# Kernel tuning notes

Measured on AMD Instinct MI355X. Metric: run time of the kernel, lower is better.

The kernel has to match this reference:

```python
import jax, jax.numpy as jnp
import numpy as np

H = 256          # hidden_size
V_IN = 29        # in_embeddng_size
V_OUT = 74       # out_embedding_size
L = 32           # encoder sequence length
STEPS = 20       # max_decoding_steps
BOS, EOS = 2, 3


def gru_cell(x, h, Wih, Whh, bih, bhh):
    # torch GRU cell: r,z,n gate order in the stacked [3H, H] weight matrices
    gi = x @ Wih.T + bih          # [3H]
    gh = h @ Whh.T + bhh          # [3H]
    ir, iz, inn = jnp.split(gi, 3)
    hr, hz, hn = jnp.split(gh, 3)
    r = jax.nn.sigmoid(ir + hr)
    z = jax.nn.sigmoid(iz + hz)
    n = jnp.tanh(inn + r * hn)
    return (1.0 - z) * n + z * h


def setup_inputs() -> dict:
    key = jax.random.key(0)
    ks = jax.random.split(key, 14)
    f = lambda k, shape: (jax.random.normal(k, shape, jnp.float32) * 0.08)
    inp = {
        "enc_input": jax.random.randint(ks[0], (1, L), 0, V_IN).astype(jnp.int32),
        "enc_emb": f(ks[1], (V_IN, H)).at[0].set(0.0),   # padding_idx=0
        "enc_Wih": f(ks[2], (3 * H, H)),
        "enc_Whh": f(ks[3], (3 * H, H)),
        "enc_bih": f(ks[4], (3 * H,)),
        "enc_bhh": f(ks[5], (3 * H,)),
        "dec_emb": f(ks[6], (V_OUT, H)).at[0].set(0.0),  # padding_idx=0
        "dec_Wih": f(ks[7], (3 * H, H)),
        "dec_Whh": f(ks[8], (3 * H, H)),
        "dec_bih": f(ks[9], (3 * H,)),
        "dec_bhh": f(ks[10], (3 * H,)),
        "fc_W": f(ks[11], (V_OUT, H)),
        "fc_b": f(ks[12], (V_OUT,)),
    }
    return inp


def reference(enc_input, enc_emb, enc_Wih, enc_Whh, enc_bih, enc_bhh,
              dec_emb, dec_Wih, dec_Whh, dec_bih, dec_bhh, fc_W, fc_b):
    # ---- encoder: embed + single-layer GRU over the sequence (batch=1) ----
    x_seq = enc_emb[enc_input[0]]                     # [L, H]
    def enc_step(h, x):
        return gru_cell(x, h, enc_Wih, enc_Whh, enc_bih, enc_bhh), None
    h0 = jnp.zeros((H,), enc_emb.dtype)
    h, _ = jax.lax.scan(enc_step, h0, x_seq)          # final hidden [H]

    # Early break is emulated by a `done` flag: once EOS is emitted, all
    # subsequent preds stay 0 (matching torch, which leaves preds zeros).
    def dec_step(carry, _):
        h, tok, done = carry
        x = dec_emb[tok]
        h2 = gru_cell(x, h, dec_Wih, dec_Whh, dec_bih, dec_bhh)
        logit = h2 @ fc_W.T + fc_b                    # [V_OUT]
        topi = jnp.argmax(logit).astype(jnp.int32)    # topk(1) == argmax
        is_eos = topi == EOS
        pred = jnp.where(done | is_eos, 0, topi)      # EOS step not recorded
        return (h2, topi, done | is_eos), pred

    init = (h, jnp.int32(BOS), jnp.bool_(False))
    _, preds = jax.lax.scan(dec_step, init, None, length=STEPS)
    return preds                                      # [20] int32
```

## Files before the change

### kernel.cpp

```cpp
#include <hip/hip_runtime.h>
#include <cmath>

#define H     256
#define H3    768
#define L     32
#define STEPS 20
#define VOUT  74
#define NWG   16
#define HW    16
#define ROWS  48
#define NITEMS (L + VOUT)

#define WS_HW    64
#define WS_EGI   1088
#define WS_DGI   (1088 + L * H3)

__device__ __forceinline__ float sigmoidf_(float x) {
    return 1.0f / (1.0f + expf(-x));
}

__device__ __forceinline__ int growf(int w, int lr) {
    int j = w * HW + (lr & 15);
    return (lr < 16) ? j : (lr < 32 ? H + j : 2 * H + j);
}

__global__ void prep(const int*   __restrict__ enc_input,
                     const float* __restrict__ enc_emb,
                     const float* __restrict__ encWih,
                     const float* __restrict__ enc_bih,
                     const float* __restrict__ dec_emb,
                     const float* __restrict__ decWih,
                     const float* __restrict__ dec_bih,
                     float* __restrict__ ws) {
    if (blockIdx.x == 0) {
        for (int k = threadIdx.x; k < 1088; k += 256) ((int*)ws)[k] = 0;
    }
    int wid  = blockIdx.x * 4 + (threadIdx.x >> 6);
    int lane = threadIdx.x & 63;
    if (wid >= NITEMS * H3) return;
    int item = wid / H3;
    int j    = wid - item * H3;

    const float* x; const float* W; const float* b; float* out;
    if (item < L) {
        x = enc_emb + enc_input[item] * H;  W = encWih + j * H;
        b = enc_bih;                        out = ws + WS_EGI + item * H3 + j;
    } else {
        int v = item - L;
        x = dec_emb + v * H;                W = decWih + j * H;
        b = dec_bih;                        out = ws + WS_DGI + v * H3 + j;
    }
    float4 w  = ((const float4*)W)[lane];
    float4 xv = ((const float4*)x)[lane];
    float s = fmaf(w.x, xv.x, fmaf(w.y, xv.y, fmaf(w.z, xv.z, w.w * xv.w)));
    #pragma unroll
    for (int m = 1; m < 64; m <<= 1) s += __shfl_xor(s, m);
    if (lane == 0) *out = s + b[j];
}

__global__ __launch_bounds__(256, 1) void gru_seq(
        const float* __restrict__ enc_Whh, const float* __restrict__ enc_bhh,
        const float* __restrict__ dec_Whh, const float* __restrict__ dec_bhh,
        const float* __restrict__ fc_W,    const float* __restrict__ fc_b,
        float* __restrict__ ws, int* __restrict__ out) {
    __shared__ float hl[1040];
    __shared__ float fcL[VOUT * 260];
    __shared__ float fb[VOUT];
    __shared__ float gh_l[ROWS];
    __shared__ float gi_l[ROWS];
    __shared__ float log_l[VOUT];
    __shared__ int   s_tok, s_done;

    const int t = threadIdx.x;
    const int w = blockIdx.x;
    unsigned long long* hw = (unsigned long long*)(ws + WS_HW);

    if (t == 0) { s_done = 0; s_tok = 2; }
    if (w == 0 && t < STEPS) out[t] = 0;
    for (int idx = t; idx < VOUT * H; idx += 256)
        fcL[(idx >> 8) * 260 + (idx & 255)] = fc_W[idx];
    if (t < VOUT) fb[t] = fc_b[t];

    const int p  = t & 3;
    const int lr = t >> 2;
    const int g  = growf(w, lr < ROWS ? lr : 0);
    float4 wE[16], wD[16];
    float bhhE = 0.f, bhhD = 0.f;
    if (t < 4 * ROWS) {
        const float* eb = enc_Whh + g * H + p * 64;
        const float* db = dec_Whh + g * H + p * 64;
        #pragma unroll
        for (int i = 0; i < 16; ++i) {
            wE[i] = *(const float4*)(eb + 4 * i);
            wD[i] = *(const float4*)(db + 4 * i);
        }
        if (p == 0) { bhhE = enc_bhh[g]; bhhD = dec_bhh[g]; }
    }

    int tok = 2;
    for (int s = 0; s <= L + STEPS; ++s) {
        {
            unsigned long long u;
            const unsigned long long* src = hw + (s & 1) * H + t;
            do {
                u = __hip_atomic_load(src, __ATOMIC_RELAXED,
                                      __HIP_MEMORY_SCOPE_AGENT);
            } while ((unsigned)u != (unsigned)s);
            float hv = __uint_as_float((unsigned)(u >> 32));
            hl[t] = hv; hl[260 + t] = hv; hl[520 + t] = hv; hl[780 + t] = hv;
        }
        __syncthreads();

        if (s >= L + 1) {
            const int G = t >> 4, li = t & 15;
            const float* hb2 = hl + (li & 3) * 260 + li * 16;
            #pragma unroll
            for (int m = 0; m < 5; ++m) {
                int r = G + (m << 4);
                if (r < VOUT) {
                    const float* fr = fcL + r * 260 + li * 16;
                    float a = 0.f;
                    #pragma unroll
                    for (int c = 0; c < 4; ++c) {
                        float4 f  = *(const float4*)(fr + 4 * c);
                        float4 h4 = *(const float4*)(hb2 + 4 * c);
                        a = fmaf(f.x, h4.x, fmaf(f.y, h4.y,
                              fmaf(f.z, h4.z, fmaf(f.w, h4.w, a))));
                    }
                    a += __shfl_xor(a, 1); a += __shfl_xor(a, 2);
                    a += __shfl_xor(a, 4); a += __shfl_xor(a, 8);
                    if (li == 0) log_l[r] = a + fb[r];
                }
            }
            __syncthreads();
            if (t < 64) {
                float v = log_l[t]; int bi = t;
                if (t < VOUT - 64) {
                    float v2 = log_l[64 + t];
                    if (v2 > v) { v = v2; bi = 64 + t; }
                }
                #pragma unroll
                for (int m = 1; m < 64; m <<= 1) {
                    float ov = __shfl_xor(v, m);
                    int   ob = __shfl_xor(bi, m);
                    if (ov > v || (ov == v && ob < bi)) { v = ov; bi = ob; }
                }
                if (t == 0) {
                    bool eos = (bi == 3);
                    if (w == 0 && !eos) out[s - (L + 1)] = bi;
                    s_tok = bi;
                    if (eos) s_done = 1;
                }
            }
            __syncthreads();
            tok = s_tok;
            if (s_done || s == L + STEPS) break;
        }

        if (t < 4 * ROWS) {
            float acc = (s < L) ? bhhE : bhhD;
            const float* hb = hl + p * 324;
            if (s < L) {
                #pragma unroll
                for (int i = 0; i < 16; ++i) {
                    float4 h4 = *(const float4*)(hb + 4 * i);
                    acc = fmaf(wE[i].x, h4.x, fmaf(wE[i].y, h4.y,
                          fmaf(wE[i].z, h4.z, fmaf(wE[i].w, h4.w, acc))));
                }
            } else {
                #pragma unroll
                for (int i = 0; i < 16; ++i) {
                    float4 h4 = *(const float4*)(hb + 4 * i);
                    acc = fmaf(wD[i].x, h4.x, fmaf(wD[i].y, h4.y,
                          fmaf(wD[i].z, h4.z, fmaf(wD[i].w, h4.w, acc))));
                }
            }
            acc += __shfl_xor(acc, 1);
            acc += __shfl_xor(acc, 2);
            if (p == 0) gh_l[lr] = acc;
        } else if (t - 4 * ROWS < ROWS) {
            int lr2 = t - 4 * ROWS;
            const float* gib = (s < L) ? (ws + WS_EGI + s * H3)
                                       : (ws + WS_DGI + tok * H3);
            gi_l[lr2] = gib[growf(w, lr2)];
        }
        __syncthreads();

        if (t < HW) {
            int gj = w * HW + t;
            float r = sigmoidf_(gi_l[t]      + gh_l[t]);
            float z = sigmoidf_(gi_l[16 + t] + gh_l[16 + t]);
            float n = tanhf    (gi_l[32 + t] + r * gh_l[32 + t]);
            float hn = (1.f - z) * n + z * hl[gj];
            unsigned long long pk =
                ((unsigned long long)__float_as_uint(hn) << 32) |
                (unsigned)(s + 1);
            __hip_atomic_store(hw + ((s + 1) & 1) * H + gj, pk,
                               __ATOMIC_RELAXED, __HIP_MEMORY_SCOPE_AGENT);
        }
    }
}

extern "C" void kernel_launch(void* const* d_in, const int* in_sizes, int n_in,
                              void* d_out, int out_size, void* d_ws, size_t ws_size,
                              hipStream_t stream) {
    const int*   enc_input = (const int*)  d_in[0];
    const float* enc_emb   = (const float*)d_in[1];
    const float* enc_Wih   = (const float*)d_in[2];
    const float* enc_Whh   = (const float*)d_in[3];
    const float* enc_bih   = (const float*)d_in[4];
    const float* enc_bhh   = (const float*)d_in[5];
    const float* dec_emb   = (const float*)d_in[6];
    const float* dec_Wih   = (const float*)d_in[7];
    const float* dec_Whh   = (const float*)d_in[8];
    const float* dec_bih   = (const float*)d_in[9];
    const float* dec_bhh   = (const float*)d_in[10];
    const float* fc_W      = (const float*)d_in[11];
    const float* fc_b      = (const float*)d_in[12];
    float* ws  = (float*)d_ws;
    int*  outp = (int*)d_out;

    hipLaunchKernelGGL(prep, dim3((NITEMS * H3 + 3) / 4), dim3(256), 0, stream,
                       enc_input, enc_emb, enc_Wih, enc_bih,
                       dec_emb, dec_Wih, dec_bih, ws);
    hipLaunchKernelGGL(gru_seq, dim3(NWG), dim3(256), 0, stream,
                       enc_Whh, enc_bhh, dec_Whh, dec_bhh, fc_W, fc_b,
                       ws, outp);
}
```

Before: 141.8 us.

## Keep FC weights in registers, preload input gates to LDS, pad hidden exchange slots

Each thread now holds its fc_W rows in registers, replacing the LDS copy of the whole matrix. The per-block slices of the precomputed input-gate projections for every encoder step and every decoder token go into LDS once, so no global read remains inside the step loop. Warp 0 now runs the argmax in parallel with the recurrent matvec done by the other warps, which removes one barrier per decoder step. Each hidden-exchange slot is padded to 64 bytes to reduce false sharing between polling blocks, at the cost of much higher register pressure (wE, wD and wF arrays) and a larger workspace clear.

```diff
diff --git a/kernel.cpp b/kernel.cpp
--- a/kernel.cpp
+++ b/kernel.cpp
@@ -11,9 +11,9 @@
 #define ROWS  48
 #define NITEMS (L + VOUT)
 
-#define WS_HW    64
-#define WS_EGI   1088
-#define WS_DGI   (1088 + L * H3)
+#define WS_HX    0
+#define WS_EGI   8192
+#define WS_DGI   (8192 + L * H3)
 
 __device__ __forceinline__ float sigmoidf_(float x) {
     return 1.0f / (1.0f + expf(-x));
@@ -33,7 +33,7 @@
                      const float* __restrict__ dec_bih,
                      float* __restrict__ ws) {
     if (blockIdx.x == 0) {
-        for (int k = threadIdx.x; k < 1088; k += 256) ((int*)ws)[k] = 0;
+        for (int k = threadIdx.x; k < 8192; k += 256) ((int*)ws)[k] = 0;
     }
     int wid  = blockIdx.x * 4 + (threadIdx.x >> 6);
     int lane = threadIdx.x & 63;
@@ -63,30 +63,37 @@
         const float* __restrict__ dec_Whh, const float* __restrict__ dec_bhh,
         const float* __restrict__ fc_W,    const float* __restrict__ fc_b,
         float* __restrict__ ws, int* __restrict__ out) {
-    __shared__ float hl[1040];
-    __shared__ float fcL[VOUT * 260];
+    __shared__ __align__(16) float hl[1040];
     __shared__ float fb[VOUT];
     __shared__ float gh_l[ROWS];
-    __shared__ float gi_l[ROWS];
+    __shared__ float egi_l[L * ROWS];
+    __shared__ float dgi_l[VOUT * ROWS];
     __shared__ float log_l[VOUT];
     __shared__ int   s_tok, s_done;
 
     const int t = threadIdx.x;
     const int w = blockIdx.x;
-    unsigned long long* hw = (unsigned long long*)(ws + WS_HW);
+    unsigned long long* hx = (unsigned long long*)(ws + WS_HX);
 
     if (t == 0) { s_done = 0; s_tok = 2; }
     if (w == 0 && t < STEPS) out[t] = 0;
-    for (int idx = t; idx < VOUT * H; idx += 256)
-        fcL[(idx >> 8) * 260 + (idx & 255)] = fc_W[idx];
     if (t < VOUT) fb[t] = fc_b[t];
-
+    for (int idx = t; idx < L * ROWS; idx += 256) {
+        int item = idx / ROWS, lr = idx - item * ROWS;
+        egi_l[idx] = ws[WS_EGI + item * H3 + growf(w, lr)];
+    }
+    for (int idx = t; idx < VOUT * ROWS; idx += 256) {
+        int item = idx / ROWS, lr = idx - item * ROWS;
+        dgi_l[idx] = ws[WS_DGI + item * H3 + growf(w, lr)];
+    }
+
+    const int m  = t - 64;
     const int p  = t & 3;
-    const int lr = t >> 2;
-    const int g  = growf(w, lr < ROWS ? lr : 0);
+    const int lr = (t >= 64) ? (m >> 2) : 0;
+    const int g  = growf(w, lr);
     float4 wE[16], wD[16];
     float bhhE = 0.f, bhhD = 0.f;
-    if (t < 4 * ROWS) {
+    if (t >= 64) {
         const float* eb = enc_Whh + g * H + p * 64;
         const float* db = dec_Whh + g * H + p * 64;
         #pragma unroll
@@ -97,11 +104,24 @@
         if (p == 0) { bhhE = enc_bhh[g]; bhhD = dec_bhh[g]; }
     }
 
+    const int rF = t >> 2;
+    float4 wF[16], wF2[16];
+    {
+        const float* fp = fc_W + rF * H + p * 64;
+        #pragma unroll
+        for (int i = 0; i < 16; ++i) wF[i] = *(const float4*)(fp + 4 * i);
+        if (t < 40) {
+            const float* fp2 = fc_W + (64 + rF) * H + p * 64;
+            #pragma unroll
+            for (int i = 0; i < 16; ++i) wF2[i] = *(const float4*)(fp2 + 4 * i);
+        }
+    }
+
     int tok = 2;
     for (int s = 0; s <= L + STEPS; ++s) {
         {
+            const unsigned long long* src = hx + ((unsigned)((s & 1) * H + t)) * 8;
             unsigned long long u;
-            const unsigned long long* src = hw + (s & 1) * H + t;
             do {
                 u = __hip_atomic_load(src, __ATOMIC_RELAXED,
                                       __HIP_MEMORY_SCOPE_AGENT);
@@ -111,38 +131,43 @@
         }
         __syncthreads();
 
-        if (s >= L + 1) {
-            const int G = t >> 4, li = t & 15;
-            const float* hb2 = hl + (li & 3) * 260 + li * 16;
+        const bool dec_out = (s >= L + 1);
+        if (dec_out) {
+            const float* hb = hl + p * 324;
+            float a = 0.f;
             #pragma unroll
-            for (int m = 0; m < 5; ++m) {
-                int r = G + (m << 4);
-                if (r < VOUT) {
-                    const float* fr = fcL + r * 260 + li * 16;
-                    float a = 0.f;
-                    #pragma unroll
-                    for (int c = 0; c < 4; ++c) {
-                        float4 f  = *(const float4*)(fr + 4 * c);
-                        float4 h4 = *(const float4*)(hb2 + 4 * c);
-                        a = fmaf(f.x, h4.x, fmaf(f.y, h4.y,
-                              fmaf(f.z, h4.z, fmaf(f.w, h4.w, a))));
-                    }
-                    a += __shfl_xor(a, 1); a += __shfl_xor(a, 2);
-                    a += __shfl_xor(a, 4); a += __shfl_xor(a, 8);
-                    if (li == 0) log_l[r] = a + fb[r];
-                }
+            for (int i = 0; i < 16; ++i) {
+                float4 h4 = *(const float4*)(hb + 4 * i);
+                a = fmaf(wF[i].x, h4.x, fmaf(wF[i].y, h4.y,
+                      fmaf(wF[i].z, h4.z, fmaf(wF[i].w, h4.w, a))));
+            }
+            a += __shfl_xor(a, 1); a += __shfl_xor(a, 2);
+            if (p == 0) log_l[rF] = a + fb[rF];
+            if (t < 40) {
+                float a2 = 0.f;
+                #pragma unroll
+                for (int i = 0; i < 16; ++i) {
+                    float4 h4 = *(const float4*)(hb + 4 * i);
+                    a2 = fmaf(wF2[i].x, h4.x, fmaf(wF2[i].y, h4.y,
+                           fmaf(wF2[i].z, h4.z, fmaf(wF2[i].w, h4.w, a2))));
+                }
+                a2 += __shfl_xor(a2, 1); a2 += __shfl_xor(a2, 2);
+                if (p == 0) log_l[64 + rF] = a2 + fb[64 + rF];
             }
             __syncthreads();
-            if (t < 64) {
+        }
+
+        if (t < 64) {
+            if (dec_out) {
                 float v = log_l[t]; int bi = t;
                 if (t < VOUT - 64) {
                     float v2 = log_l[64 + t];
                     if (v2 > v) { v = v2; bi = 64 + t; }
                 }
                 #pragma unroll
-                for (int m = 1; m < 64; m <<= 1) {
-                    float ov = __shfl_xor(v, m);
-                    int   ob = __shfl_xor(bi, m);
+                for (int mm = 1; mm < 64; mm <<= 1) {
+                    float ov = __shfl_xor(v, mm);
+                    int   ob = __shfl_xor(bi, mm);
                     if (ov > v || (ov == v && ob < bi)) { v = ov; bi = ob; }
                 }
                 if (t == 0) {
@@ -152,12 +177,7 @@
                     if (eos) s_done = 1;
                 }
             }
-            __syncthreads();
-            tok = s_tok;
-            if (s_done || s == L + STEPS) break;
-        }
-
-        if (t < 4 * ROWS) {
+        } else {
             float acc = (s < L) ? bhhE : bhhD;
             const float* hb = hl + p * 324;
             if (s < L) {
@@ -177,26 +197,26 @@
             }
             acc += __shfl_xor(acc, 1);
             acc += __shfl_xor(acc, 2);
-            if (p == 0) gh_l[lr] = acc;
-        } else if (t - 4 * ROWS < ROWS) {
-            int lr2 = t - 4 * ROWS;
-            const float* gib = (s < L) ? (ws + WS_EGI + s * H3)
-                                       : (ws + WS_DGI + tok * H3);
-            gi_l[lr2] = gib[growf(w, lr2)];
+            if (p == 0) gh_l[m >> 2] = acc;
         }
         __syncthreads();
 
+        if (dec_out) {
+            tok = s_tok;
+            if (s_done || s == L + STEPS) break;
+        }
+
         if (t < HW) {
-            int gj = w * HW + t;
-            float r = sigmoidf_(gi_l[t]      + gh_l[t]);
-            float z = sigmoidf_(gi_l[16 + t] + gh_l[16 + t]);
-            float n = tanhf    (gi_l[32 + t] + r * gh_l[32 + t]);
-            float hn = (1.f - z) * n + z * hl[gj];
+            const float* gi = (s < L) ? (egi_l + s * ROWS) : (dgi_l + tok * ROWS);
+            float r = sigmoidf_(gi[t]      + gh_l[t]);
+            float z = sigmoidf_(gi[16 + t] + gh_l[16 + t]);
+            float n = tanhf    (gi[32 + t] + r * gh_l[32 + t]);
+            float hn = (1.f - z) * n + z * hl[w * HW + t];
             unsigned long long pk =
                 ((unsigned long long)__float_as_uint(hn) << 32) |
                 (unsigned)(s + 1);
-            __hip_atomic_store(hw + ((s + 1) & 1) * H + gj, pk,
-                               __ATOMIC_RELAXED, __HIP_MEMORY_SCOPE_AGENT);
+            __hip_atomic_store(hx + ((unsigned)(((s + 1) & 1) * H + w * HW + t)) * 8,
+                               pk, __ATOMIC_RELAXED, __HIP_MEMORY_SCOPE_AGENT);
         }
     }
 }
```

New measurement: 153.8 us. 1.08x slower.
